# Kernel optimization log

Measured on AMD Instinct MI355X. Metric: run time of the kernel, lower is better.

## Reference

```python
import jax, jax.numpy as jnp
import numpy as np

N = 50000      # nodes
E = 800000     # edges (avg degree 16)
IN = 128       # in_features
OUT = 64       # out_features
NEG_SLOPE = 0.2


def setup_inputs() -> dict:
    key = jax.random.key(0)
    ks = jax.random.split(key, 6)
    x = jax.random.normal(ks[0], (N, IN), dtype=jnp.float32)
    edge_src = jax.random.randint(ks[1], (E,), 0, N, dtype=jnp.int32)  # row i of adj
    edge_dst = jax.random.randint(ks[2], (E,), 0, N, dtype=jnp.int32)  # col j of adj
    stdv = 1.0 / np.sqrt(OUT)
    W = jax.random.uniform(ks[3], (IN, OUT), jnp.float32, -stdv, stdv)
    a = jax.random.uniform(ks[4], (2 * OUT, 1), jnp.float32, -stdv, stdv)
    bias = jax.random.uniform(ks[5], (OUT,), jnp.float32, -stdv, stdv)
    return {"x": x, "W": W, "a": a, "bias": bias,
            "edge_src": edge_src, "edge_dst": edge_dst}


def reference(x, W, a, bias, edge_src, edge_dst):
    # h = input @ weight + bias    [N, OUT]
    h = x @ W + bias
    # Per-node attention halves: Wh1[i] + Wh2[j] == (e = Wh1 + Wh2.T)[i, j]
    Wh1 = h @ a[:OUT, 0]   # [N]
    Wh2 = h @ a[OUT:, 0]   # [N]
    # Edge-centric scores only where adj is nonzero (mirrors e.sparse_mask(adj))
    e = jax.nn.leaky_relu(Wh1[edge_src] + Wh2[edge_dst], NEG_SLOPE)  # [E]
    # Sparse softmax over dim=1 -> segment softmax grouped by source row
    emax = jax.ops.segment_max(e, edge_src, num_segments=N)          # [N]
    ex = jnp.exp(e - emax[edge_src])                                 # [E]
    denom = jax.ops.segment_sum(ex, edge_src, num_segments=N)        # [N]
    alpha = ex / denom[edge_src]                                     # [E]
    # out[i] = sum_j alpha_ij * h[j]  (sparse attention @ h)
    out = jax.ops.segment_sum(alpha[:, None] * h[edge_dst], edge_src,
                              num_segments=N)                        # [N, OUT]
    return out
```

## Files before the change

### kernel.cpp

```cpp
#include <hip/hip_runtime.h>
#include <math.h>


typedef unsigned long long u64;
typedef unsigned int u32;
typedef unsigned short u16;
typedef __attribute__((ext_vector_type(8))) short bf16x8;
typedef __attribute__((ext_vector_type(4))) float f32x4;

namespace {
constexpr int NN   = 50000;
constexpr int EE   = 800000;
constexpr int INF_ = 128;
constexpr int OUTF = 64;
constexpr float NEG_SLOPE = 0.2f;
constexpr int MAXDEG = 64;

constexpr int NBUCK   = 196;
constexpr int BSTRIDE = 16;
constexpr int BCAP    = 4608;
constexpr int S1_CHUNK  = 2048;
constexpr int S1_BLOCKS = (EE + S1_CHUNK - 1) / S1_CHUNK;
constexpr int GEMM_BLOCKS = (NN + 127) / 128;
constexpr int K1_BLOCKS = S1_BLOCKS + GEMM_BLOCKS;
constexpr int AGG_BLOCKS = (NN + 63) / 64;
}

static __device__ __forceinline__ u16 bf16rne(float v) {
    u32 u = __builtin_bit_cast(u32, v);
    return (u16)((u + 0x7fffu + ((u >> 16) & 1u)) >> 16);
}
static __device__ __forceinline__ float bf2f(u16 b) {
    return __builtin_bit_cast(float, (u32)b << 16);
}
static __device__ __forceinline__ u32 pack2bf(float a, float b) {
    return (u32)bf16rne(a) | ((u32)bf16rne(b) << 16);
}

__global__ __launch_bounds__(256)
void gat_prep(const float* __restrict__ W, int* __restrict__ bcnt_g,
              u32* __restrict__ Whi_g, u32* __restrict__ Wlo_g)
{
    const int tid = threadIdx.x;
    if (blockIdx.x == 0) {
        for (int i = tid; i < NBUCK * BSTRIDE; i += 256) bcnt_g[i] = 0;
        return;
    }
    const int idx    = (blockIdx.x - 1) * 256 + tid;
    const int lane_s = idx & 63;
    const int kt_s   = (idx >> 6) & 3;
    const int nt_s   = idx >> 8;
    const int n  = nt_s * 16 + (lane_s & 15);
    const int k0 = kt_s * 32 + (lane_s >> 4) * 8;
    u32 hw[4], lw[4];
#pragma unroll
    for (int jp = 0; jp < 4; ++jp) {
        const float va = W[(k0 + 2*jp    ) * OUTF + n];
        const float vb = W[(k0 + 2*jp + 1) * OUTF + n];
        const u16 hA = bf16rne(va); const u16 lA = bf16rne(va - bf2f(hA));
        const u16 hB = bf16rne(vb); const u16 lB = bf16rne(vb - bf2f(hB));
        hw[jp] = (u32)hA | ((u32)hB << 16);
        lw[jp] = (u32)lA | ((u32)lB << 16);
    }
    const int off = ((nt_s * 4 + kt_s) * 64 + lane_s) * 4;
    *(uint4*)&Whi_g[off] = make_uint4(hw[0], hw[1], hw[2], hw[3]);
    *(uint4*)&Wlo_g[off] = make_uint4(lw[0], lw[1], lw[2], lw[3]);
}

__global__ __launch_bounds__(256)
void gat_fused(const float* __restrict__ x,
               const u32* __restrict__ Whi_g, const u32* __restrict__ Wlo_g,
               const float* __restrict__ av, const float* __restrict__ bias,
               const int* __restrict__ esrc, const int* __restrict__ edst,
               u32* __restrict__ h16, float* __restrict__ wh1,
               float* __restrict__ wh2, int* __restrict__ bcnt_g,
               u64* __restrict__ bdata)
{
    __shared__ u64 smem[2368];
    const int id  = blockIdx.x;
    const int tid = threadIdx.x;
    const int ridx = id >> 1;
    const bool is_gemm = (id & 1) == 0;

    if (!is_gemm) {
        u64* s_pairs = smem;
        int* s_bcnt  = (int*)((char*)smem + 16384);
        int* s_scan  = s_bcnt + NBUCK;
        int* s_goff  = s_scan + NBUCK;

        for (int i = tid; i < NBUCK; i += 256) s_bcnt[i] = 0;
        __syncthreads();

        const int e0  = ridx * S1_CHUNK;
        const int tot = (EE - e0) < S1_CHUNK ? (EE - e0) : S1_CHUNK;

        int mb[8], mp[8]; u64 mv[8]; int nmine = 0;
#pragma unroll
        for (int k = 0; k < 8; ++k) {
            const int e = e0 + tid + k * 256;
            if (e < e0 + tot) {
                const int s = esrc[e], d = edst[e];
                const int b = s >> 8;
                mb[nmine] = b;
                mp[nmine] = atomicAdd(&s_bcnt[b], 1);
                mv[nmine] = ((u64)(u32)d << 32) | (u32)s;
                ++nmine;
            }
        }
        __syncthreads();
        if (tid < NBUCK) s_scan[tid] = s_bcnt[tid];
        __syncthreads();
        for (int off = 1; off < NBUCK; off <<= 1) {
            int v = 0;
            if (tid < NBUCK && tid >= off) v = s_scan[tid - off];
            __syncthreads();
            if (tid < NBUCK && tid >= off) s_scan[tid] += v;
            __syncthreads();
        }
        if (tid < NBUCK) {
            const int c = s_bcnt[tid];
            s_goff[tid] = c > 0 ? atomicAdd(&bcnt_g[tid * BSTRIDE], c) : 0;
        }
        __syncthreads();
        for (int k = 0; k < nmine; ++k) {
            const int b = mb[k];
            s_pairs[s_scan[b] - s_bcnt[b] + mp[k]] = mv[k];
        }
        __syncthreads();
        for (int i = tid; i < tot; i += 256) {
            const u64 p = s_pairs[i];
            const int s = (int)(u32)(p & 0xffffffffull);
            const int b = s >> 8;
            const int g = s_goff[b] + (i - (s_scan[b] - s_bcnt[b]));
            if (g < BCAP) bdata[(size_t)b * BCAP + g] = p;
        }
        return;
    }

    const int lane = tid & 63;
    const int w    = tid >> 6;
    const int n15  = lane & 15;
    const int quad = lane >> 4;
    const int node0  = ridx * 128;
    const int nodeA0 = node0 + w * 32;

    f32x4 acc[2][4];
#pragma unroll
    for (int mt = 0; mt < 2; ++mt)
#pragma unroll
        for (int nt = 0; nt < 4; ++nt) acc[mt][nt] = (f32x4)(0.f);

    for (int kt = 0; kt < 4; ++kt) {
        bf16x8 Ahi[2], Alo[2];
#pragma unroll
        for (int mt = 0; mt < 2; ++mt) {
            const int node = nodeA0 + mt * 16 + n15;
            float v[8] = {0.f,0.f,0.f,0.f,0.f,0.f,0.f,0.f};
            if (node < NN) {
                const float4* xr = (const float4*)(x + (size_t)node * INF_ + kt * 32 + quad * 8);
                const float4 p = xr[0], q = xr[1];
                v[0]=p.x; v[1]=p.y; v[2]=p.z; v[3]=p.w;
                v[4]=q.x; v[5]=q.y; v[6]=q.z; v[7]=q.w;
            }
#pragma unroll
            for (int j = 0; j < 8; ++j) {
                const u16 hb = bf16rne(v[j]);
                const u16 lb = bf16rne(v[j] - bf2f(hb));
                Ahi[mt][j] = (short)hb;
                Alo[mt][j] = (short)lb;
            }
        }
#pragma unroll
        for (int nt = 0; nt < 4; ++nt) {
            const int off = ((nt * 4 + kt) * 64 + lane) * 4;
            const bf16x8 Bhi = *(const bf16x8*)&Whi_g[off];
            const bf16x8 Blo = *(const bf16x8*)&Wlo_g[off];
#pragma unroll
            for (int mt = 0; mt < 2; ++mt) {
                acc[mt][nt] = __builtin_amdgcn_mfma_f32_16x16x32_bf16(Ahi[mt], Bhi, acc[mt][nt], 0, 0, 0);
                acc[mt][nt] = __builtin_amdgcn_mfma_f32_16x16x32_bf16(Ahi[mt], Blo, acc[mt][nt], 0, 0, 0);
                acc[mt][nt] = __builtin_amdgcn_mfma_f32_16x16x32_bf16(Alo[mt], Bhi, acc[mt][nt], 0, 0, 0);
            }
        }
    }

#pragma unroll
    for (int mt = 0; mt < 2; ++mt) {
        float p1[4] = {0.f,0.f,0.f,0.f}, p2[4] = {0.f,0.f,0.f,0.f};
        float hv[4][4];
#pragma unroll
        for (int nt = 0; nt < 4; ++nt) {
            const int feat = nt * 16 + n15;
            const float bv = bias[feat];
            const float A1 = av[feat];
            const float A2 = av[OUTF + feat];
#pragma unroll
            for (int r = 0; r < 4; ++r) {
                const float d = acc[mt][nt][r] + bv;
                hv[nt][r] = d;
                p1[r] += d * A1;
                p2[r] += d * A2;
            }
        }
#pragma unroll
        for (int r = 0; r < 4; ++r) {
            p1[r] += __shfl_xor(p1[r], 1); p1[r] += __shfl_xor(p1[r], 2);
            p1[r] += __shfl_xor(p1[r], 4); p1[r] += __shfl_xor(p1[r], 8);
            p2[r] += __shfl_xor(p2[r], 1); p2[r] += __shfl_xor(p2[r], 2);
            p2[r] += __shfl_xor(p2[r], 4); p2[r] += __shfl_xor(p2[r], 8);
        }
#pragma unroll
        for (int r = 0; r < 4; ++r) {
            float pk[4];
#pragma unroll
            for (int nt = 0; nt < 4; ++nt) pk[nt] = __shfl_xor(hv[nt][r], 1);
            const int node = nodeA0 + mt * 16 + quad * 4 + r;
            if (node < NN) {
                if ((n15 & 1) == 0) {
#pragma unroll
                    for (int nt = 0; nt < 4; ++nt)
                        h16[(size_t)node * 32 + nt * 8 + (n15 >> 1)] =
                            pack2bf(hv[nt][r], pk[nt]);
                }
                if (n15 == 0) { wh1[node] = p1[r]; wh2[node] = p2[r]; }
            }
        }
    }
}

__global__ __launch_bounds__(256)
void gat_agg(const int* __restrict__ bcnt_g, const u64* __restrict__ bdata,
             const float* __restrict__ wh1, const float* __restrict__ wh2,
             const u32* __restrict__ h16, float* __restrict__ out)
{
    __shared__ u64 l_ad[64 * 65];
    __shared__ int l_cnt[64];
    const int tid    = threadIdx.x;
    const int bid    = blockIdx.x;
    const int node0  = bid << 6;
    const int bucket = bid >> 2;

    if (tid < 64) l_cnt[tid] = 0;
    __syncthreads();

    int n = bcnt_g[bucket * BSTRIDE];
    n = n > BCAP ? BCAP : n;
    for (int i = tid; i < n; i += 256) {
        const u64 p = bdata[(size_t)bucket * BCAP + i];
        const int s  = (int)(u32)(p & 0xffffffffull);
        const int ln = s - node0;
        if (ln >= 0 && ln < 64) {
            const int pos = atomicAdd(&l_cnt[ln], 1);
            if (pos < MAXDEG)
                ((u32*)&l_ad[ln * 65 + pos])[1] = (u32)(p >> 32);
        }
    }
    __syncthreads();

    const int lane = tid & 63;
    const int qw   = (tid >> 6) * 4 + (lane >> 4);
    const int f    = lane & 15;

#pragma unroll
    for (int nl = 0; nl < 4; ++nl) {
        const int li   = qw + 16 * nl;
        const int node = node0 + li;
        int deg = l_cnt[li];
        deg = deg > MAXDEG ? MAXDEG : deg;
        const float w1 = (node < NN) ? wh1[node] : 0.f;

        float el[4]; int dl[4];
        float m = -INFINITY;
#pragma unroll
        for (int k = 0; k < 4; ++k) {
            const int slot = f + 16 * k;
            int d = (int)((u32*)&l_ad[li * 65 + slot])[1];
            d = (slot < deg) ? d : 0;
            dl[k] = d;
            float v = w1 + wh2[d];
            v = v > 0.f ? v : NEG_SLOPE * v;
            el[k] = (slot < deg) ? v : -INFINITY;
            m = fmaxf(m, el[k]);
        }
        m = fmaxf(m, __shfl_xor(m, 1)); m = fmaxf(m, __shfl_xor(m, 2));
        m = fmaxf(m, __shfl_xor(m, 4)); m = fmaxf(m, __shfl_xor(m, 8));
        float ex[4], s = 0.f;
#pragma unroll
        for (int k = 0; k < 4; ++k) {
            ex[k] = (f + 16 * k < deg) ? __expf(el[k] - m) : 0.f;
            s += ex[k];
        }
        s += __shfl_xor(s, 1); s += __shfl_xor(s, 2);
        s += __shfl_xor(s, 4); s += __shfl_xor(s, 8);
        const float inv = (deg > 0) ? 1.f / s : 0.f;
#pragma unroll
        for (int k = 0; k < 4; ++k) {
            const u32 ab = __builtin_bit_cast(u32, ex[k] * inv);
            l_ad[li * 65 + f + 16 * k] = (u64)ab | ((u64)(u32)dl[k] << 32);
        }
    }
    __syncthreads();

    const int c  = f & 7;
    const int eh = f >> 3;
#pragma unroll
    for (int nl = 0; nl < 4; ++nl) {
        const int li   = qw + 16 * nl;
        const int node = node0 + li;
        int deg = l_cnt[li];
        deg = deg > MAXDEG ? MAXDEG : deg;
        const int base = li * 65;
        float a8[8] = {0.f,0.f,0.f,0.f,0.f,0.f,0.f,0.f};
        for (int j0 = 0; j0 < deg; j0 += 16) {
            u64 ad[8]; uint4 vv[8];
#pragma unroll
            for (int k = 0; k < 8; ++k)
                ad[k] = l_ad[base + j0 + 2 * k + eh];
#pragma unroll
            for (int k = 0; k < 8; ++k) {
                const u32 d = (u32)(ad[k] >> 32);
                vv[k] = *(const uint4*)&h16[(size_t)d * 32 + c * 4];
            }
#define BF_LO(u) __builtin_bit_cast(float, (u) << 16)
#define BF_HI(u) __builtin_bit_cast(float, (u) & 0xffff0000u)
#pragma unroll
            for (int k = 0; k < 8; ++k) {
                const float a = __builtin_bit_cast(float, (u32)ad[k]);
                a8[0] += a * BF_LO(vv[k].x); a8[1] += a * BF_HI(vv[k].x);
                a8[2] += a * BF_LO(vv[k].y); a8[3] += a * BF_HI(vv[k].y);
                a8[4] += a * BF_LO(vv[k].z); a8[5] += a * BF_HI(vv[k].z);
                a8[6] += a * BF_LO(vv[k].w); a8[7] += a * BF_HI(vv[k].w);
            }
#undef BF_LO
#undef BF_HI
        }
#pragma unroll
        for (int i = 0; i < 8; ++i) a8[i] += __shfl_xor(a8[i], 8);
        if (node < NN)
            *(float4*)&out[(size_t)node * OUTF + c * 8 + eh * 4] =
                make_float4(a8[eh*4+0], a8[eh*4+1], a8[eh*4+2], a8[eh*4+3]);
    }
}

extern "C" void kernel_launch(void* const* d_in, const int* in_sizes, int n_in,
                              void* d_out, int out_size, void* d_ws, size_t ws_size,
                              hipStream_t stream)
{
    const float* x    = (const float*)d_in[0];
    const float* W    = (const float*)d_in[1];
    const float* av   = (const float*)d_in[2];
    const float* bias = (const float*)d_in[3];
    const int*   esrc = (const int*)d_in[4];
    const int*   edst = (const int*)d_in[5];
    float* out = (float*)d_out;

    u32*   h16    = (u32*)d_ws;
    float* wh1    = (float*)(h16 + (size_t)NN * 32);
    float* wh2    = wh1 + NN;
    int*   bcnt_g = (int*)(wh2 + NN);
    u32*   Whi_g  = (u32*)(bcnt_g + NBUCK * BSTRIDE);
    u32*   Wlo_g  = Whi_g + 4096;
    u64*   bdata  = (u64*)(Wlo_g + 4096);

    gat_prep<<<5, 256, 0, stream>>>(W, bcnt_g, Whi_g, Wlo_g);
    gat_fused<<<K1_BLOCKS, 256, 0, stream>>>(
        x, Whi_g, Wlo_g, av, bias, esrc, edst, h16, wh1, wh2, bcnt_g, bdata);
    gat_agg<<<AGG_BLOCKS, 256, 0, stream>>>(bcnt_g, bdata, wh1, wh2, h16, out);
}
```

Measured before the change: 123.2 us.

## Replace global bucket atomics with per-chunk slots and fold weight prep into GEMM

```diff
diff --git a/kernel.cpp b/kernel.cpp
--- a/kernel.cpp
+++ b/kernel.cpp
@@ -17,12 +17,12 @@
 constexpr int MAXDEG = 64;
 
 constexpr int NBUCK   = 196;
-constexpr int BSTRIDE = 16;
-constexpr int BCAP    = 4608;
 constexpr int S1_CHUNK  = 2048;
-constexpr int S1_BLOCKS = (EE + S1_CHUNK - 1) / S1_CHUNK;
+constexpr int NCHUNK    = (EE + S1_CHUNK - 1) / S1_CHUNK;
+constexpr int CCAP      = 40;
+constexpr int BSLOTS    = NCHUNK * CCAP;
 constexpr int GEMM_BLOCKS = (NN + 127) / 128;
-constexpr int K1_BLOCKS = S1_BLOCKS + GEMM_BLOCKS;
+constexpr int K1_BLOCKS = NCHUNK + GEMM_BLOCKS;
 constexpr int AGG_BLOCKS = (NN + 63) / 64;
 }
 
@@ -38,45 +38,14 @@
 }
 
 __global__ __launch_bounds__(256)
-void gat_prep(const float* __restrict__ W, int* __restrict__ bcnt_g,
-              u32* __restrict__ Whi_g, u32* __restrict__ Wlo_g)
-{
-    const int tid = threadIdx.x;
-    if (blockIdx.x == 0) {
-        for (int i = tid; i < NBUCK * BSTRIDE; i += 256) bcnt_g[i] = 0;
-        return;
-    }
-    const int idx    = (blockIdx.x - 1) * 256 + tid;
-    const int lane_s = idx & 63;
-    const int kt_s   = (idx >> 6) & 3;
-    const int nt_s   = idx >> 8;
-    const int n  = nt_s * 16 + (lane_s & 15);
-    const int k0 = kt_s * 32 + (lane_s >> 4) * 8;
-    u32 hw[4], lw[4];
-#pragma unroll
-    for (int jp = 0; jp < 4; ++jp) {
-        const float va = W[(k0 + 2*jp    ) * OUTF + n];
-        const float vb = W[(k0 + 2*jp + 1) * OUTF + n];
-        const u16 hA = bf16rne(va); const u16 lA = bf16rne(va - bf2f(hA));
-        const u16 hB = bf16rne(vb); const u16 lB = bf16rne(vb - bf2f(hB));
-        hw[jp] = (u32)hA | ((u32)hB << 16);
-        lw[jp] = (u32)lA | ((u32)lB << 16);
-    }
-    const int off = ((nt_s * 4 + kt_s) * 64 + lane_s) * 4;
-    *(uint4*)&Whi_g[off] = make_uint4(hw[0], hw[1], hw[2], hw[3]);
-    *(uint4*)&Wlo_g[off] = make_uint4(lw[0], lw[1], lw[2], lw[3]);
-}
-
-__global__ __launch_bounds__(256)
-void gat_fused(const float* __restrict__ x,
-               const u32* __restrict__ Whi_g, const u32* __restrict__ Wlo_g,
+void gat_fused(const float* __restrict__ x, const float* __restrict__ W,
                const float* __restrict__ av, const float* __restrict__ bias,
                const int* __restrict__ esrc, const int* __restrict__ edst,
                u32* __restrict__ h16, float* __restrict__ wh1,
-               float* __restrict__ wh2, int* __restrict__ bcnt_g,
+               float* __restrict__ wh2, u16* __restrict__ cnt2d,
                u64* __restrict__ bdata)
 {
-    __shared__ u64 smem[2368];
+    __shared__ u64 smem[4096];
     const int id  = blockIdx.x;
     const int tid = threadIdx.x;
     const int ridx = id >> 1;
@@ -86,7 +55,6 @@
         u64* s_pairs = smem;
         int* s_bcnt  = (int*)((char*)smem + 16384);
         int* s_scan  = s_bcnt + NBUCK;
-        int* s_goff  = s_scan + NBUCK;
 
         for (int i = tid; i < NBUCK; i += 256) s_bcnt[i] = 0;
         __syncthreads();
@@ -117,11 +85,6 @@
             if (tid < NBUCK && tid >= off) s_scan[tid] += v;
             __syncthreads();
         }
-        if (tid < NBUCK) {
-            const int c = s_bcnt[tid];
-            s_goff[tid] = c > 0 ? atomicAdd(&bcnt_g[tid * BSTRIDE], c) : 0;
-        }
-        __syncthreads();
         for (int k = 0; k < nmine; ++k) {
             const int b = mb[k];
             s_pairs[s_scan[b] - s_bcnt[b] + mp[k]] = mv[k];
@@ -131,11 +94,44 @@
             const u64 p = s_pairs[i];
             const int s = (int)(u32)(p & 0xffffffffull);
             const int b = s >> 8;
-            const int g = s_goff[b] + (i - (s_scan[b] - s_bcnt[b]));
-            if (g < BCAP) bdata[(size_t)b * BCAP + g] = p;
+            const int pos = i - (s_scan[b] - s_bcnt[b]);
+            if (pos < CCAP)
+                bdata[(size_t)b * BSLOTS + ridx * CCAP + pos] = p;
+        }
+        if (tid < NBUCK) {
+            int c = s_bcnt[tid];
+            c = c > CCAP ? CCAP : c;
+            cnt2d[(size_t)tid * NCHUNK + ridx] = (u16)c;
         }
         return;
     }
+
+    u32* Whi = (u32*)smem;
+    u32* Wlo = Whi + 4096;
+
+#pragma unroll
+    for (int i = 0; i < 4; ++i) {
+        const int idx    = tid * 4 + i;
+        const int lane_s = idx & 63;
+        const int kt_s   = (idx >> 6) & 3;
+        const int nt_s   = idx >> 8;
+        const int n  = nt_s * 16 + (lane_s & 15);
+        const int k0 = kt_s * 32 + (lane_s >> 4) * 8;
+        u32 hw[4], lw[4];
+#pragma unroll
+        for (int jp = 0; jp < 4; ++jp) {
+            const float va = W[(k0 + 2*jp    ) * OUTF + n];
+            const float vb = W[(k0 + 2*jp + 1) * OUTF + n];
+            const u16 hA = bf16rne(va); const u16 lA = bf16rne(va - bf2f(hA));
+            const u16 hB = bf16rne(vb); const u16 lB = bf16rne(vb - bf2f(hB));
+            hw[jp] = (u32)hA | ((u32)hB << 16);
+            lw[jp] = (u32)lA | ((u32)lB << 16);
+        }
+        const int off = ((nt_s * 4 + kt_s) * 64 + lane_s) * 4;
+        *(uint4*)&Whi[off] = make_uint4(hw[0], hw[1], hw[2], hw[3]);
+        *(uint4*)&Wlo[off] = make_uint4(lw[0], lw[1], lw[2], lw[3]);
+    }
+    __syncthreads();
 
     const int lane = tid & 63;
     const int w    = tid >> 6;
@@ -173,8 +169,8 @@
 #pragma unroll
         for (int nt = 0; nt < 4; ++nt) {
             const int off = ((nt * 4 + kt) * 64 + lane) * 4;
-            const bf16x8 Bhi = *(const bf16x8*)&Whi_g[off];
-            const bf16x8 Blo = *(const bf16x8*)&Wlo_g[off];
+            const bf16x8 Bhi = *(const bf16x8*)&Whi[off];
+            const bf16x8 Blo = *(const bf16x8*)&Wlo[off];
 #pragma unroll
             for (int mt = 0; mt < 2; ++mt) {
                 acc[mt][nt] = __builtin_amdgcn_mfma_f32_16x16x32_bf16(Ahi[mt], Bhi, acc[mt][nt], 0, 0, 0);
@@ -228,8 +224,8 @@
     }
 }
 
-__global__ __launch_bounds__(256)
-void gat_agg(const int* __restrict__ bcnt_g, const u64* __restrict__ bdata,
+__global__ __launch_bounds__(512)
+void gat_agg(const u16* __restrict__ cnt2d, const u64* __restrict__ bdata,
              const float* __restrict__ wh1, const float* __restrict__ wh2,
              const u32* __restrict__ h16, float* __restrict__ out)
 {
@@ -243,16 +239,21 @@
     if (tid < 64) l_cnt[tid] = 0;
     __syncthreads();
 
-    int n = bcnt_g[bucket * BSTRIDE];
-    n = n > BCAP ? BCAP : n;
-    for (int i = tid; i < n; i += 256) {
-        const u64 p = bdata[(size_t)bucket * BCAP + i];
-        const int s  = (int)(u32)(p & 0xffffffffull);
-        const int ln = s - node0;
-        if (ln >= 0 && ln < 64) {
-            const int pos = atomicAdd(&l_cnt[ln], 1);
-            if (pos < MAXDEG)
-                ((u32*)&l_ad[ln * 65 + pos])[1] = (u32)(p >> 32);
+    {
+        const int wv   = tid >> 6;
+        const int lane = tid & 63;
+        for (int c = wv; c < NCHUNK; c += 8) {
+            const int n_c = cnt2d[(size_t)bucket * NCHUNK + c];
+            if (lane < n_c) {
+                const u64 p = bdata[(size_t)bucket * BSLOTS + c * CCAP + lane];
+                const int s  = (int)(u32)(p & 0xffffffffull);
+                const int ln = s - node0;
+                if (ln >= 0 && ln < 64) {
+                    const int pos = atomicAdd(&l_cnt[ln], 1);
+                    if (pos < MAXDEG)
+                        ((u32*)&l_ad[ln * 65 + pos])[1] = (u32)(p >> 32);
+                }
+            }
         }
     }
     __syncthreads();
@@ -262,8 +263,8 @@
     const int f    = lane & 15;
 
 #pragma unroll
-    for (int nl = 0; nl < 4; ++nl) {
-        const int li   = qw + 16 * nl;
+    for (int nl = 0; nl < 2; ++nl) {
+        const int li   = qw + 32 * nl;
         const int node = node0 + li;
         int deg = l_cnt[li];
         deg = deg > MAXDEG ? MAXDEG : deg;
@@ -304,8 +305,8 @@
     const int c  = f & 7;
     const int eh = f >> 3;
 #pragma unroll
-    for (int nl = 0; nl < 4; ++nl) {
-        const int li   = qw + 16 * nl;
+    for (int nl = 0; nl < 2; ++nl) {
+        const int li   = qw + 32 * nl;
         const int node = node0 + li;
         int deg = l_cnt[li];
         deg = deg > MAXDEG ? MAXDEG : deg;
@@ -357,13 +358,10 @@
     u32*   h16    = (u32*)d_ws;
     float* wh1    = (float*)(h16 + (size_t)NN * 32);
     float* wh2    = wh1 + NN;
-    int*   bcnt_g = (int*)(wh2 + NN);
-    u32*   Whi_g  = (u32*)(bcnt_g + NBUCK * BSTRIDE);
-    u32*   Wlo_g  = Whi_g + 4096;
-    u64*   bdata  = (u64*)(Wlo_g + 4096);
-
-    gat_prep<<<5, 256, 0, stream>>>(W, bcnt_g, Whi_g, Wlo_g);
+    u16*   cnt2d  = (u16*)(wh2 + NN);
+    u64*   bdata  = (u64*)((char*)d_ws + (size_t)16 * 1024 * 1024);
+
     gat_fused<<<K1_BLOCKS, 256, 0, stream>>>(
-        x, Whi_g, Wlo_g, av, bias, esrc, edst, h16, wh1, wh2, bcnt_g, bdata);
-    gat_agg<<<AGG_BLOCKS, 256, 0, stream>>>(bcnt_g, bdata, wh1, wh2, h16, out);
-}
+        x, W, av, bias, esrc, edst, h16, wh1, wh2, cnt2d, bdata);
+    gat_agg<<<AGG_BLOCKS, 512, 0, stream>>>(cnt2d, bdata, wh1, wh2, h16, out);
+}
```

After: 178.0 us. 44.6% more time.

## Bucket edges per 64-node block and convert W inside GEMM blocks

Applied to the files above, without the earlier changes.

```diff
diff --git a/kernel.cpp b/kernel.cpp
--- a/kernel.cpp
+++ b/kernel.cpp
@@ -16,9 +16,9 @@
 constexpr float NEG_SLOPE = 0.2f;
 constexpr int MAXDEG = 64;
 
-constexpr int NBUCK   = 196;
+constexpr int NBUCK   = 784;
 constexpr int BSTRIDE = 16;
-constexpr int BCAP    = 4608;
+constexpr int BCAP    = 1280;
 constexpr int S1_CHUNK  = 2048;
 constexpr int S1_BLOCKS = (EE + S1_CHUNK - 1) / S1_CHUNK;
 constexpr int GEMM_BLOCKS = (NN + 127) / 128;
@@ -38,45 +38,14 @@
 }
 
 __global__ __launch_bounds__(256)
-void gat_prep(const float* __restrict__ W, int* __restrict__ bcnt_g,
-              u32* __restrict__ Whi_g, u32* __restrict__ Wlo_g)
-{
-    const int tid = threadIdx.x;
-    if (blockIdx.x == 0) {
-        for (int i = tid; i < NBUCK * BSTRIDE; i += 256) bcnt_g[i] = 0;
-        return;
-    }
-    const int idx    = (blockIdx.x - 1) * 256 + tid;
-    const int lane_s = idx & 63;
-    const int kt_s   = (idx >> 6) & 3;
-    const int nt_s   = idx >> 8;
-    const int n  = nt_s * 16 + (lane_s & 15);
-    const int k0 = kt_s * 32 + (lane_s >> 4) * 8;
-    u32 hw[4], lw[4];
-#pragma unroll
-    for (int jp = 0; jp < 4; ++jp) {
-        const float va = W[(k0 + 2*jp    ) * OUTF + n];
-        const float vb = W[(k0 + 2*jp + 1) * OUTF + n];
-        const u16 hA = bf16rne(va); const u16 lA = bf16rne(va - bf2f(hA));
-        const u16 hB = bf16rne(vb); const u16 lB = bf16rne(vb - bf2f(hB));
-        hw[jp] = (u32)hA | ((u32)hB << 16);
-        lw[jp] = (u32)lA | ((u32)lB << 16);
-    }
-    const int off = ((nt_s * 4 + kt_s) * 64 + lane_s) * 4;
-    *(uint4*)&Whi_g[off] = make_uint4(hw[0], hw[1], hw[2], hw[3]);
-    *(uint4*)&Wlo_g[off] = make_uint4(lw[0], lw[1], lw[2], lw[3]);
-}
-
-__global__ __launch_bounds__(256)
-void gat_fused(const float* __restrict__ x,
-               const u32* __restrict__ Whi_g, const u32* __restrict__ Wlo_g,
+void gat_fused(const float* __restrict__ x, const float* __restrict__ W,
                const float* __restrict__ av, const float* __restrict__ bias,
                const int* __restrict__ esrc, const int* __restrict__ edst,
                u32* __restrict__ h16, float* __restrict__ wh1,
                float* __restrict__ wh2, int* __restrict__ bcnt_g,
                u64* __restrict__ bdata)
 {
-    __shared__ u64 smem[2368];
+    __shared__ u64 smem[4096];
     const int id  = blockIdx.x;
     const int tid = threadIdx.x;
     const int ridx = id >> 1;
@@ -84,11 +53,12 @@
 
     if (!is_gemm) {
         u64* s_pairs = smem;
-        int* s_bcnt  = (int*)((char*)smem + 16384);
-        int* s_scan  = s_bcnt + NBUCK;
-        int* s_goff  = s_scan + NBUCK;
-
-        for (int i = tid; i < NBUCK; i += 256) s_bcnt[i] = 0;
+        int* s_cnt   = (int*)((char*)smem + 16384);
+        int* s_base  = s_cnt + NBUCK;
+        int* s_goff  = s_base + NBUCK;
+        int* s_part  = s_goff + NBUCK;
+
+        for (int i = tid; i < NBUCK; i += 256) s_cnt[i] = 0;
         __syncthreads();
 
         const int e0  = ridx * S1_CHUNK;
@@ -100,42 +70,77 @@
             const int e = e0 + tid + k * 256;
             if (e < e0 + tot) {
                 const int s = esrc[e], d = edst[e];
-                const int b = s >> 8;
+                const int b = s >> 6;
                 mb[nmine] = b;
-                mp[nmine] = atomicAdd(&s_bcnt[b], 1);
+                mp[nmine] = atomicAdd(&s_cnt[b], 1);
                 mv[nmine] = ((u64)(u32)d << 32) | (u32)s;
                 ++nmine;
             }
         }
         __syncthreads();
-        if (tid < NBUCK) s_scan[tid] = s_bcnt[tid];
-        __syncthreads();
-        for (int off = 1; off < NBUCK; off <<= 1) {
+        int c4[4] = {0,0,0,0};
+        if (tid < 196) {
+#pragma unroll
+            for (int i = 0; i < 4; ++i) c4[i] = s_cnt[tid * 4 + i];
+        }
+        s_part[tid] = c4[0] + c4[1] + c4[2] + c4[3];
+        __syncthreads();
+        for (int off = 1; off < 256; off <<= 1) {
             int v = 0;
-            if (tid < NBUCK && tid >= off) v = s_scan[tid - off];
+            if (tid >= off) v = s_part[tid - off];
             __syncthreads();
-            if (tid < NBUCK && tid >= off) s_scan[tid] += v;
+            if (tid >= off) s_part[tid] += v;
             __syncthreads();
         }
-        if (tid < NBUCK) {
-            const int c = s_bcnt[tid];
-            s_goff[tid] = c > 0 ? atomicAdd(&bcnt_g[tid * BSTRIDE], c) : 0;
-        }
-        __syncthreads();
-        for (int k = 0; k < nmine; ++k) {
-            const int b = mb[k];
-            s_pairs[s_scan[b] - s_bcnt[b] + mp[k]] = mv[k];
-        }
+        if (tid < 196) {
+            int run = (tid > 0) ? s_part[tid - 1] : 0;
+#pragma unroll
+            for (int i = 0; i < 4; ++i) {
+                const int b = tid * 4 + i;
+                s_base[b] = run;
+                s_goff[b] = c4[i] > 0 ? atomicAdd(&bcnt_g[b * BSTRIDE], c4[i]) : 0;
+                run += c4[i];
+            }
+        }
+        __syncthreads();
+        for (int k = 0; k < nmine; ++k)
+            s_pairs[s_base[mb[k]] + mp[k]] = mv[k];
         __syncthreads();
         for (int i = tid; i < tot; i += 256) {
             const u64 p = s_pairs[i];
-            const int s = (int)(u32)(p & 0xffffffffull);
-            const int b = s >> 8;
-            const int g = s_goff[b] + (i - (s_scan[b] - s_bcnt[b]));
+            const int b = (int)(u32)(p & 0xffffffffull) >> 6;
+            const int g = s_goff[b] + (i - s_base[b]);
             if (g < BCAP) bdata[(size_t)b * BCAP + g] = p;
         }
         return;
     }
+
+    u32* Whi = (u32*)smem;
+    u32* Wlo = Whi + 4096;
+
+#pragma unroll
+    for (int i = 0; i < 4; ++i) {
+        const int idx    = tid * 4 + i;
+        const int lane_s = idx & 63;
+        const int kt_s   = (idx >> 6) & 3;
+        const int nt_s   = idx >> 8;
+        const int n  = nt_s * 16 + (lane_s & 15);
+        const int k0 = kt_s * 32 + (lane_s >> 4) * 8;
+        u32 hw[4], lw[4];
+#pragma unroll
+        for (int jp = 0; jp < 4; ++jp) {
+            const float va = W[(k0 + 2*jp    ) * OUTF + n];
+            const float vb = W[(k0 + 2*jp + 1) * OUTF + n];
+            const u16 hA = bf16rne(va); const u16 lA = bf16rne(va - bf2f(hA));
+            const u16 hB = bf16rne(vb); const u16 lB = bf16rne(vb - bf2f(hB));
+            hw[jp] = (u32)hA | ((u32)hB << 16);
+            lw[jp] = (u32)lA | ((u32)lB << 16);
+        }
+        const int off = ((nt_s * 4 + kt_s) * 64 + lane_s) * 4;
+        *(uint4*)&Whi[off] = make_uint4(hw[0], hw[1], hw[2], hw[3]);
+        *(uint4*)&Wlo[off] = make_uint4(lw[0], lw[1], lw[2], lw[3]);
+    }
+    __syncthreads();
 
     const int lane = tid & 63;
     const int w    = tid >> 6;
@@ -173,8 +178,8 @@
 #pragma unroll
         for (int nt = 0; nt < 4; ++nt) {
             const int off = ((nt * 4 + kt) * 64 + lane) * 4;
-            const bf16x8 Bhi = *(const bf16x8*)&Whi_g[off];
-            const bf16x8 Blo = *(const bf16x8*)&Wlo_g[off];
+            const bf16x8 Bhi = *(const bf16x8*)&Whi[off];
+            const bf16x8 Blo = *(const bf16x8*)&Wlo[off];
 #pragma unroll
             for (int mt = 0; mt < 2; ++mt) {
                 acc[mt][nt] = __builtin_amdgcn_mfma_f32_16x16x32_bf16(Ahi[mt], Bhi, acc[mt][nt], 0, 0, 0);
@@ -235,25 +240,21 @@
 {
     __shared__ u64 l_ad[64 * 65];
     __shared__ int l_cnt[64];
-    const int tid    = threadIdx.x;
-    const int bid    = blockIdx.x;
-    const int node0  = bid << 6;
-    const int bucket = bid >> 2;
+    const int tid   = threadIdx.x;
+    const int bid   = blockIdx.x;
+    const int node0 = bid << 6;
 
     if (tid < 64) l_cnt[tid] = 0;
     __syncthreads();
 
-    int n = bcnt_g[bucket * BSTRIDE];
+    int n = bcnt_g[bid * BSTRIDE];
     n = n > BCAP ? BCAP : n;
     for (int i = tid; i < n; i += 256) {
-        const u64 p = bdata[(size_t)bucket * BCAP + i];
-        const int s  = (int)(u32)(p & 0xffffffffull);
-        const int ln = s - node0;
-        if (ln >= 0 && ln < 64) {
-            const int pos = atomicAdd(&l_cnt[ln], 1);
-            if (pos < MAXDEG)
-                ((u32*)&l_ad[ln * 65 + pos])[1] = (u32)(p >> 32);
-        }
+        const u64 p = bdata[(size_t)bid * BCAP + i];
+        const int ln = (int)(u32)(p & 63u);
+        const int pos = atomicAdd(&l_cnt[ln], 1);
+        if (pos < MAXDEG)
+            ((u32*)&l_ad[ln * 65 + pos])[1] = (u32)(p >> 32);
     }
     __syncthreads();
 
@@ -358,12 +359,10 @@
     float* wh1    = (float*)(h16 + (size_t)NN * 32);
     float* wh2    = wh1 + NN;
     int*   bcnt_g = (int*)(wh2 + NN);
-    u32*   Whi_g  = (u32*)(bcnt_g + NBUCK * BSTRIDE);
-    u32*   Wlo_g  = Whi_g + 4096;
-    u64*   bdata  = (u64*)(Wlo_g + 4096);
-
-    gat_prep<<<5, 256, 0, stream>>>(W, bcnt_g, Whi_g, Wlo_g);
+    u64*   bdata  = (u64*)(bcnt_g + NBUCK * BSTRIDE);
+
+    hipMemsetAsync(bcnt_g, 0, NBUCK * BSTRIDE * sizeof(int), stream);
     gat_fused<<<K1_BLOCKS, 256, 0, stream>>>(
-        x, Whi_g, Wlo_g, av, bias, esrc, edst, h16, wh1, wh2, bcnt_g, bdata);
+        x, W, av, bias, esrc, edst, h16, wh1, wh2, bcnt_g, bdata);
     gat_agg<<<AGG_BLOCKS, 256, 0, stream>>>(bcnt_g, bdata, wh1, wh2, h16, out);
 }
```

Result: slower. 130.4 us (+5.9%).
